# Performance work log

Measured on AMD Instinct MI355X. Metric: run time of the kernel, lower is better.

Reference implementation:

```python
import jax, jax.numpy as jnp
import numpy as np

TEMPERATURE = 10.0
EPS = 1e-12  # torch F.normalize eps


def setup_inputs() -> dict:
    key = jax.random.key(0)
    k1, k2 = jax.random.split(key)
    B, D = 8192, 1024
    text_embeddings = jax.random.normal(k1, (B, D), dtype=jnp.float32)
    image_embeddings = jax.random.normal(k2, (B, D), dtype=jnp.float32)
    bias = jnp.zeros((1,), dtype=jnp.float32)
    return {
        "text_embeddings": text_embeddings,
        "image_embeddings": image_embeddings,
        "bias": bias,
    }


def _normalize(x):
    # matches torch F.normalize(p=2, dim=1): x / max(||x||, eps)
    norm = jnp.linalg.norm(x, axis=-1, keepdims=True)
    return x / jnp.maximum(norm, EPS)


def reference(text_embeddings, image_embeddings, bias):
    B = text_embeddings.shape[0]
    img_n = _normalize(image_embeddings)   # [B, D]
    txt_n = _normalize(text_embeddings)    # [B, D]
    # similarity[i, j] = <img_i, txt_j>
    sim = jnp.einsum('id,jd->ij', img_n, txt_n)          # [B, B]
    logits = sim * (-TEMPERATURE) + bias[0]
    labels = 2.0 * jnp.eye(B, dtype=logits.dtype) - 1.0   # +1 diag, -1 off-diag
    # loss_ij = log(1/(1+exp(label*logit))) = -softplus(label*logit)
    total_loss = -jnp.sum(jax.nn.softplus(labels * logits))
    return -(total_loss / B)
```

## Files before the change

kernel.cpp:

```cpp
#include <hip/hip_runtime.h>
#include <stdint.h>
#include <stddef.h>

#define NROWS 8192
#define DIM   1024
#define RB    512
#define TEMP  10.0f

#define BM 256
#define BN 256
#define BK 128
#define NT (DIM / BK)

typedef __attribute__((ext_vector_type(8))) int i32x8;
typedef __attribute__((ext_vector_type(16))) float floatx16;

__device__ __forceinline__ void load16_lds(const unsigned char* g, unsigned char* l) {
    __builtin_amdgcn_global_load_lds(
        (__attribute__((address_space(1))) void*)(g),
        (__attribute__((address_space(3))) void*)(l),
        16, 0, 0);
}

__device__ __forceinline__ unsigned fp4q(float x) {
    float a = fabsf(x);
    a = fminf(a, 6.0f);
    unsigned c = (unsigned)(a >= 0.25f) + (unsigned)(a >= 0.75f)
               + (unsigned)(a >= 1.25f) + (unsigned)(a >= 1.75f)
               + (unsigned)(a >= 2.5f)  + (unsigned)(a >= 3.5f)
               + (unsigned)(a >= 5.0f);
    return c | ((__float_as_uint(x) >> 28) & 8u);
}


__global__ __launch_bounds__(256) void normalize_kernel(
    const float* __restrict__ img, const float* __restrict__ txt,
    unsigned char* __restrict__ imgq, unsigned char* __restrict__ txtq,
    float* __restrict__ out)
{
    __shared__ __align__(16) unsigned short sc[4][256];
    const int t = threadIdx.x;
    const int lane = t & 63, wave = t >> 6;
    const int gw = blockIdx.x * 4 + wave;
    const float* src = (gw < NROWS) ? img + (size_t)gw * DIM
                                    : txt + (size_t)(gw - NROWS) * DIM;
    float4 v[4];
    float ss = 0.f;
#pragma unroll
    for (int c = 0; c < 4; c++) {
        v[c] = ((const float4*)src)[lane + 64 * c];
        ss += v[c].x * v[c].x + v[c].y * v[c].y + v[c].z * v[c].z + v[c].w * v[c].w;
    }
#pragma unroll
    for (int off = 32; off; off >>= 1) ss += __shfl_xor(ss, off);
    const float scale = 32.0f / fmaxf(sqrtf(ss), 1e-12f);
#pragma unroll
    for (int c = 0; c < 4; c++) {
        unsigned p = fp4q(v[c].x * scale)
                   | (fp4q(v[c].y * scale) << 4)
                   | (fp4q(v[c].z * scale) << 8)
                   | (fp4q(v[c].w * scale) << 12);
        sc[wave][c * 64 + lane] = (unsigned short)p;
    }
    __syncthreads();
    if (t < 128) {
        const int rr = t & 3, k = t >> 2;
        const int gr0 = blockIdx.x * 4;
        unsigned char* dq = (gr0 < NROWS) ? imgq : txtq;
        const int r = (gr0 < NROWS ? gr0 : gr0 - NROWS) + rr;
        const int4 d = *(const int4*)&sc[rr][k * 8];
        const int it = k >> 2, ks = (k >> 1) & 1, fh = k & 1;
        *(int4*)(dq + (size_t)it * 524288 + (size_t)((r >> 5) * 2048
                 + ks * 1024 + fh * 512 + (r & 31) * 16)) = d;
    }
    if (gw == 0 && lane == 0) out[0] = 0.f;
}

__global__ __launch_bounds__(512, 2) void simloss_kernel(
    const unsigned char* __restrict__ An,
    const unsigned char* __restrict__ Bn,
    const float* __restrict__ bias,
    float* __restrict__ out)
{
    __shared__ __align__(16) unsigned char As[8 * 16384];
    __shared__ float red[4][8];

    const int t = threadIdx.x;
    const int lane = t & 63;
    const int wave = t >> 6;

    const int bid = blockIdx.x;
    const int blockM = bid >> 3;
    const int n0 = bid & 3 ? (bid & 7) : (bid & 7);

    {
        const unsigned char* gA = An + (size_t)blockM * 16384 + t * 16;
#pragma unroll
        for (int it = 0; it < 8; it++) {
#pragma unroll
            for (int j = 0; j < 2; j++)
                load16_lds(gA + (size_t)it * 524288 + j * 8192,
                           As + it * 16384 + j * 8192 + t * 16);
        }
    }
    asm volatile("s_waitcnt vmcnt(0)" ::: "memory");
    __syncthreads();

    const int waveM = (wave >> 2) * 128;
    const int waveN = (wave & 3) * 64;
    const int rgA = (wave >> 2) * 4;
    const int cgB = (wave & 3) * 2;
    const int fr = lane & 31;
    const int fh = lane >> 5;

    i32x8 aT[2][4], bT[2][2];
#pragma unroll
    for (int p = 0; p < 2; p++) {
#pragma unroll
        for (int mi = 0; mi < 4; mi++) aT[p][mi] = (i32x8)0;
#pragma unroll
        for (int ni = 0; ni < 2; ni++) bT[p][ni] = (i32x8)0;
    }

#define LOADA(P, IT, KS)                                                        \
    {                                                                           \
        _Pragma("unroll")                                                       \
        for (int mi_ = 0; mi_ < 4; mi_++)                                       \
            *(int4*)&aT[P][mi_] = *(const int4*)(As + (IT) * 16384              \
                + (rgA + mi_) * 2048 + (KS) * 1024 + lane * 16);                \
    }
#define LOADB(P, N, IT, KS)                                                     \
    {                                                                           \
        _Pragma("unroll")                                                       \
        for (int ni_ = 0; ni_ < 2; ni_++)                                       \
            *(int4*)&bT[P][ni_] = *(const int4*)(Bn + (size_t)(IT) * 524288     \
                + (size_t)(((N) * 8 + cgB + ni_) * 2048 + (KS) * 1024           \
                           + lane * 16));                                       \
    }

    LOADA(0, 0, 0);
    LOADB(0, n0, 0, 0);

    const float bv = bias[0];
    const float c1 = -TEMP * 1.4426950408889634f / 1024.0f;
    const float c0 = bv * 1.4426950408889634f;

#pragma unroll
    for (int k = 0; k < 4; k++) {
        const int n = n0 + 8 * k;
        floatx16 acc[4][2];
#pragma unroll
        for (int mi = 0; mi < 4; mi++)
#pragma unroll
            for (int ni = 0; ni < 2; ni++)
                acc[mi][ni] = (floatx16)(0.f);

#pragma unroll
        for (int ss = 0; ss < 16; ss++) {
            const int s = k * 16 + ss;
            const int p = s & 1;
            if (s < 63) {
                const int s1 = s + 1;
                const int it1 = (s1 >> 1) & 7;
                const int ks1 = s1 & 1;
                const int n1 = n0 + 8 * (s1 >> 4);
                LOADA(p ^ 1, it1, ks1);
                LOADB(p ^ 1, n1, it1, ks1);
            }
#pragma unroll
            for (int mi = 0; mi < 4; mi++)
#pragma unroll
                for (int ni = 0; ni < 2; ni++)
                    acc[mi][ni] = __builtin_amdgcn_mfma_scale_f32_32x32x64_f8f6f4(
                        aT[p][mi], bT[p][ni], acc[mi][ni],
                        4, 4,
                        0, 0x7f7f7f7f,
                        0, 0x7f7f7f7f);
        }

        float accP = 0.f, accQ = 0.f, accD = 0.f;
        const int gi0 = blockM * BM + waveM + 4 * fh;
        const int gj0 = n * BN + waveN + fr;
#pragma unroll
        for (int mi = 0; mi < 4; mi++) {
#pragma unroll
            for (int ni = 0; ni < 2; ni++) {
#pragma unroll
                for (int reg = 0; reg < 16; reg++) {
                    float sv = acc[mi][ni][reg];
                    float w = fmaf(sv, c1, c0);
                    float e2 = __builtin_amdgcn_exp2f(-fabsf(w));
                    accP += __builtin_amdgcn_logf(1.0f + e2);
                    accP = fmaf(0.5f, fabsf(w), accP);
                    accQ += sv;
                }
            }
        }
        const bool diagblk = (n == blockM);
        if (diagblk) {
#pragma unroll
            for (int mi = 0; mi < 4; mi++)
#pragma unroll
                for (int ni = 0; ni < 2; ni++)
#pragma unroll
                    for (int reg = 0; reg < 16; reg++) {
                        int ig = gi0 + mi * 32 + (reg & 3) + 8 * (reg >> 2);
                        int jg = gj0 + ni * 32;
                        if (ig == jg) accD += acc[mi][ni][reg];
                    }
        }
#pragma unroll
        for (int off = 32; off; off >>= 1) {
            accP += __shfl_xor(accP, off);
            accQ += __shfl_xor(accQ, off);
            accD += __shfl_xor(accD, off);
        }
        if (lane == 0) {
            float wcon = fmaf(0.6931471805599453f, accP,
                              fmaf(5.0f / 1024.0f, accQ,
                                   diagblk ? (-TEMP / 1024.0f) * accD : 0.f));
            red[k][wave] = wcon;
        }
        __syncthreads();
        if (t == 0) {
            float sum = 0.f;
#pragma unroll
            for (int w = 0; w < 8; w++) sum += red[k][w];
            sum += -32768.0f * bv;
            if (diagblk) sum += 256.0f * bv;
            atomicAdd(out, sum * (1.0f / 8192.0f));
        }
    }
#undef LOADA
#undef LOADB
}

extern "C" void kernel_launch(void* const* d_in, const int* in_sizes, int n_in,
                              void* d_out, int out_size, void* d_ws, size_t ws_size,
                              hipStream_t stream) {
    const float* txt = (const float*)d_in[0];
    const float* img = (const float*)d_in[1];
    const float* bias = (const float*)d_in[2];
    float* out = (float*)d_out;

    unsigned char* imgq = (unsigned char*)d_ws;
    unsigned char* txtq = imgq + (size_t)NROWS * RB;

    normalize_kernel<<<dim3(2 * NROWS / 4), dim3(256), 0, stream>>>(
        img, txt, imgq, txtq, out);

    simloss_kernel<<<dim3(256), dim3(512), 0, stream>>>(
        imgq, txtq, bias, out);
}
```

Before: 146.1 us.

## Halve M tile to 128 rows, double grid, and pipeline B loads per K-step

```diff
diff --git a/kernel.cpp b/kernel.cpp
--- a/kernel.cpp
+++ b/kernel.cpp
@@ -7,11 +7,10 @@
 #define RB    512
 #define TEMP  10.0f
 
-#define BM 256
+#define BM 128
 #define BN 256
-#define BK 128
-#define NT (DIM / BK)
-
+
+typedef __attribute__((ext_vector_type(4))) int i32x4;
 typedef __attribute__((ext_vector_type(8))) int i32x8;
 typedef __attribute__((ext_vector_type(16))) float floatx16;
 
@@ -30,6 +29,10 @@
                + (unsigned)(a >= 2.5f)  + (unsigned)(a >= 3.5f)
                + (unsigned)(a >= 5.0f);
     return c | ((__float_as_uint(x) >> 28) & 8u);
+}
+
+__device__ __forceinline__ i32x8 op8u(i32x4 lo) {
+    return __builtin_shufflevector(lo, lo, 0, 1, 2, 3, -1, -1, -1, -1);
 }
 
 
@@ -76,14 +79,13 @@
     if (gw == 0 && lane == 0) out[0] = 0.f;
 }
 
-__global__ __launch_bounds__(512, 2) void simloss_kernel(
+__global__ __launch_bounds__(512, 4) void simloss_kernel(
     const unsigned char* __restrict__ An,
     const unsigned char* __restrict__ Bn,
     const float* __restrict__ bias,
     float* __restrict__ out)
 {
-    __shared__ __align__(16) unsigned char As[8 * 16384];
-    __shared__ float red[4][8];
+    __shared__ __align__(16) unsigned char As[8 * 8192];
 
     const int t = threadIdx.x;
     const int lane = t & 63;
@@ -91,115 +93,124 @@
 
     const int bid = blockIdx.x;
     const int blockM = bid >> 3;
-    const int n0 = bid & 3 ? (bid & 7) : (bid & 7);
+    const int n0 = bid & 7;
 
     {
-        const unsigned char* gA = An + (size_t)blockM * 16384 + t * 16;
-#pragma unroll
-        for (int it = 0; it < 8; it++) {
-#pragma unroll
-            for (int j = 0; j < 2; j++)
-                load16_lds(gA + (size_t)it * 524288 + j * 8192,
-                           As + it * 16384 + j * 8192 + t * 16);
-        }
+        const unsigned char* gA = An + (size_t)blockM * 8192 + t * 16;
+#pragma unroll
+        for (int it = 0; it < 8; it++)
+            load16_lds(gA + (size_t)it * 524288, As + it * 8192 + t * 16);
     }
     asm volatile("s_waitcnt vmcnt(0)" ::: "memory");
     __syncthreads();
 
-    const int waveM = (wave >> 2) * 128;
-    const int waveN = (wave & 3) * 64;
-    const int rgA = (wave >> 2) * 4;
+    const int rgA = (wave >> 2) * 2;
     const int cgB = (wave & 3) * 2;
     const int fr = lane & 31;
     const int fh = lane >> 5;
-
-    i32x8 aT[2][4], bT[2][2];
-#pragma unroll
-    for (int p = 0; p < 2; p++) {
-#pragma unroll
-        for (int mi = 0; mi < 4; mi++) aT[p][mi] = (i32x8)0;
-#pragma unroll
-        for (int ni = 0; ni < 2; ni++) bT[p][ni] = (i32x8)0;
-    }
-
-#define LOADA(P, IT, KS)                                                        \
-    {                                                                           \
-        _Pragma("unroll")                                                       \
-        for (int mi_ = 0; mi_ < 4; mi_++)                                       \
-            *(int4*)&aT[P][mi_] = *(const int4*)(As + (IT) * 16384              \
-                + (rgA + mi_) * 2048 + (KS) * 1024 + lane * 16);                \
-    }
-#define LOADB(P, N, IT, KS)                                                     \
-    {                                                                           \
-        _Pragma("unroll")                                                       \
-        for (int ni_ = 0; ni_ < 2; ni_++)                                       \
-            *(int4*)&bT[P][ni_] = *(const int4*)(Bn + (size_t)(IT) * 524288     \
-                + (size_t)(((N) * 8 + cgB + ni_) * 2048 + (KS) * 1024           \
-                           + lane * 16));                                       \
-    }
-
-    LOADA(0, 0, 0);
-    LOADB(0, n0, 0, 0);
+    const int vA0 = rgA * 2048 + lane * 16;
 
     const float bv = bias[0];
     const float c1 = -TEMP * 1.4426950408889634f / 1024.0f;
     const float c0 = bv * 1.4426950408889634f;
 
-#pragma unroll
-    for (int k = 0; k < 4; k++) {
+    for (int k = 0; k < 4; ++k) {
         const int n = n0 + 8 * k;
-        floatx16 acc[4][2];
-#pragma unroll
-        for (int mi = 0; mi < 4; mi++)
+        const unsigned char* gB = Bn + (size_t)((n * 8 + cgB) * 2048 + lane * 16);
+
+        floatx16 acc[2][2];
+#pragma unroll
+        for (int mi = 0; mi < 2; mi++)
 #pragma unroll
             for (int ni = 0; ni < 2; ni++)
                 acc[mi][ni] = (floatx16)(0.f);
 
-#pragma unroll
-        for (int ss = 0; ss < 16; ss++) {
-            const int s = k * 16 + ss;
-            const int p = s & 1;
-            if (s < 63) {
-                const int s1 = s + 1;
-                const int it1 = (s1 >> 1) & 7;
-                const int ks1 = s1 & 1;
-                const int n1 = n0 + 8 * (s1 >> 4);
-                LOADA(p ^ 1, it1, ks1);
-                LOADB(p ^ 1, n1, it1, ks1);
+        i32x4 b0[4], b1[4];
+#pragma unroll
+        for (int j = 0; j < 4; j++)
+            b0[j] = *(const i32x4*)(gB + (j >> 1) * 1024 + (j & 1) * 2048);
+
+        int vA = vA0;
+        for (int pp = 0; pp < 4; ++pp) {
+            {
+                i32x4 a[2][2];
+#pragma unroll
+                for (int ks = 0; ks < 2; ks++)
+#pragma unroll
+                    for (int mi = 0; mi < 2; mi++)
+                        a[ks][mi] = *(const i32x4*)&As[vA + mi * 2048 + ks * 1024];
+                const unsigned char* gB1 = gB + 524288;
+#pragma unroll
+                for (int j = 0; j < 4; j++)
+                    b1[j] = *(const i32x4*)(gB1 + (j >> 1) * 1024 + (j & 1) * 2048);
+#pragma unroll
+                for (int ks = 0; ks < 2; ks++)
+#pragma unroll
+                    for (int mi = 0; mi < 2; mi++)
+#pragma unroll
+                        for (int ni = 0; ni < 2; ni++)
+                            acc[mi][ni] = __builtin_amdgcn_mfma_scale_f32_32x32x64_f8f6f4(
+                                op8u(a[ks][mi]), op8u(b0[ks * 2 + ni]), acc[mi][ni],
+                                4, 4,
+                                0, 0x7f7f7f7f,
+                                0, 0x7f7f7f7f);
             }
-#pragma unroll
-            for (int mi = 0; mi < 4; mi++)
-#pragma unroll
-                for (int ni = 0; ni < 2; ni++)
-                    acc[mi][ni] = __builtin_amdgcn_mfma_scale_f32_32x32x64_f8f6f4(
-                        aT[p][mi], bT[p][ni], acc[mi][ni],
-                        4, 4,
-                        0, 0x7f7f7f7f,
-                        0, 0x7f7f7f7f);
+            vA += 8192;
+            gB += 2 * 524288;
+            {
+                i32x4 a[2][2];
+#pragma unroll
+                for (int ks = 0; ks < 2; ks++)
+#pragma unroll
+                    for (int mi = 0; mi < 2; mi++)
+                        a[ks][mi] = *(const i32x4*)&As[vA + mi * 2048 + ks * 1024];
+                if (pp < 3) {
+#pragma unroll
+                    for (int j = 0; j < 4; j++)
+                        b0[j] = *(const i32x4*)(gB + (j >> 1) * 1024 + (j & 1) * 2048);
+                }
+#pragma unroll
+                for (int ks = 0; ks < 2; ks++)
+#pragma unroll
+                    for (int mi = 0; mi < 2; mi++)
+#pragma unroll
+                        for (int ni = 0; ni < 2; ni++)
+                            acc[mi][ni] = __builtin_amdgcn_mfma_scale_f32_32x32x64_f8f6f4(
+                                op8u(a[ks][mi]), op8u(b1[ks * 2 + ni]), acc[mi][ni],
+                                4, 4,
+                                0, 0x7f7f7f7f,
+                                0, 0x7f7f7f7f);
+            }
+            vA += 8192;
         }
 
         float accP = 0.f, accQ = 0.f, accD = 0.f;
-        const int gi0 = blockM * BM + waveM + 4 * fh;
-        const int gj0 = n * BN + waveN + fr;
-#pragma unroll
-        for (int mi = 0; mi < 4; mi++) {
+#pragma unroll
+        for (int mi = 0; mi < 2; mi++) {
 #pragma unroll
             for (int ni = 0; ni < 2; ni++) {
 #pragma unroll
-                for (int reg = 0; reg < 16; reg++) {
-                    float sv = acc[mi][ni][reg];
-                    float w = fmaf(sv, c1, c0);
-                    float e2 = __builtin_amdgcn_exp2f(-fabsf(w));
-                    accP += __builtin_amdgcn_logf(1.0f + e2);
-                    accP = fmaf(0.5f, fabsf(w), accP);
-                    accQ += sv;
+                for (int g = 0; g < 2; g++) {
+                    float prod = 1.0f;
+#pragma unroll
+                    for (int r8 = 0; r8 < 8; r8++) {
+                        float sv = acc[mi][ni][g * 8 + r8];
+                        float w = fmaf(sv, c1, c0);
+                        float aw = fabsf(w);
+                        prod *= 1.0f + __builtin_amdgcn_exp2f(-aw);
+                        accP = fmaf(0.5f, aw, accP);
+                        accQ += sv;
+                    }
+                    accP += __builtin_amdgcn_logf(prod);
                 }
             }
         }
-        const bool diagblk = (n == blockM);
+        const bool diagblk = (n == (blockM >> 1));
         if (diagblk) {
-#pragma unroll
-            for (int mi = 0; mi < 4; mi++)
+            const int gi0 = blockM * BM + (wave >> 2) * 64 + 4 * fh;
+            const int gj0 = n * BN + (wave & 3) * 64 + fr;
+#pragma unroll
+            for (int mi = 0; mi < 2; mi++)
 #pragma unroll
                 for (int ni = 0; ni < 2; ni++)
 #pragma unroll
@@ -219,20 +230,11 @@
             float wcon = fmaf(0.6931471805599453f, accP,
                               fmaf(5.0f / 1024.0f, accQ,
                                    diagblk ? (-TEMP / 1024.0f) * accD : 0.f));
-            red[k][wave] = wcon;
-        }
-        __syncthreads();
-        if (t == 0) {
-            float sum = 0.f;
-#pragma unroll
-            for (int w = 0; w < 8; w++) sum += red[k][w];
-            sum += -32768.0f * bv;
-            if (diagblk) sum += 256.0f * bv;
-            atomicAdd(out, sum * (1.0f / 8192.0f));
-        }
-    }
-#undef LOADA
-#undef LOADB
+            if (wave == 0)
+                wcon += fmaf(-16384.0f, bv, diagblk ? 128.0f * bv : 0.f);
+            atomicAdd(out, wcon * (1.0f / 8192.0f));
+        }
+    }
 }
 
 extern "C" void kernel_launch(void* const* d_in, const int* in_sizes, int n_in,
@@ -249,6 +251,6 @@
     normalize_kernel<<<dim3(2 * NROWS / 4), dim3(256), 0, stream>>>(
         img, txt, imgq, txtq, out);
 
-    simloss_kernel<<<dim3(256), dim3(512), 0, stream>>>(
+    simloss_kernel<<<dim3((NROWS / BM) * 8), dim3(512), 0, stream>>>(
         imgq, txtq, bias, out);
 }
```

After: 442.1 us. 203% more time.
